# Performance work log

Hardware: AMD Instinct MI355X
Metric: run time of the kernel (lower is better)

The kernel has to match this reference:

```python
import jax, jax.numpy as jnp
import numpy as np

SHAPES = ((64, 64), (32, 32), (16, 16), (8, 8))
HEADS, LV, P = 8, 4, 8


def _ln(x, g, b, eps=1e-5):
    m = x.mean(-1, keepdims=True)
    v = ((x - m) ** 2).mean(-1, keepdims=True)
    return (x - m) * jax.lax.rsqrt(v + eps) * g + b


def _sample_level(v, H, W, loc):
    # v: [B, heads, H*W, hd] value for one level; loc: [B, L, heads, P, 2] in [0,1]
    # Matches F.grid_sample(mode='bilinear', padding_mode='zeros', align_corners=False)
    x = loc[..., 0] * W - 0.5
    y = loc[..., 1] * H - 0.5
    x0 = jnp.floor(x)
    y0 = jnp.floor(y)
    B, L, hds, Pn = x.shape
    acc = 0.0
    for dx, dy in ((0, 0), (1, 0), (0, 1), (1, 1)):
        xi = x0 + dx
        yi = y0 + dy
        w = (1.0 - jnp.abs(x - xi)) * (1.0 - jnp.abs(y - yi))
        valid = (xi >= 0) & (xi < W) & (yi >= 0) & (yi < H)
        idx = (jnp.clip(yi, 0, H - 1) * W + jnp.clip(xi, 0, W - 1)).astype(jnp.int32)
        idx_r = idx.transpose(0, 2, 1, 3).reshape(B, hds, L * Pn)  # [B,heads,L*P]
        g = jnp.take_along_axis(v, idx_r[..., None], axis=2)  # [B,heads,L*P,hd]
        g = g.reshape(B, hds, L, Pn, -1).transpose(0, 2, 1, 3, 4)  # [B,L,heads,P,hd]
        acc = acc + (w * valid.astype(w.dtype))[..., None] * g
    return acc


def setup_inputs() -> dict:
    key = jax.random.key(0)
    ks = iter(jax.random.split(key, 64))
    B, d, depth, dff = 2, 256, 6, 1024
    inp = {}
    for i, (H, W) in enumerate(SHAPES):
        inp[f"src{i}"] = jax.random.normal(next(ks), (B, d, H, W), jnp.float32)
        inp[f"pos{i}"] = jax.random.normal(next(ks), (B, d, H, W), jnp.float32)
    s = 0.02
    off_dim = HEADS * LV * P * 2  # 512
    aw_dim = HEADS * LV * P  # 256
    inp["level_embed"] = jax.random.normal(next(ks), (LV, d), jnp.float32)
    inp["W_off"] = jax.random.normal(next(ks), (depth, d, off_dim), jnp.float32) * s
    inp["b_off"] = jax.random.normal(next(ks), (depth, off_dim), jnp.float32) * 0.5
    inp["W_attn"] = jax.random.normal(next(ks), (depth, d, aw_dim), jnp.float32) * s
    inp["b_attn"] = jnp.zeros((depth, aw_dim), jnp.float32)
    inp["W_val"] = jax.random.normal(next(ks), (depth, d, d), jnp.float32) * s
    inp["b_val"] = jnp.zeros((depth, d), jnp.float32)
    inp["W_out"] = jax.random.normal(next(ks), (depth, d, d), jnp.float32) * s
    inp["b_out"] = jnp.zeros((depth, d), jnp.float32)
    inp["ln1_g"] = jnp.ones((depth, d), jnp.float32)
    inp["ln1_b"] = jnp.zeros((depth, d), jnp.float32)
    inp["W1"] = jax.random.normal(next(ks), (depth, d, dff), jnp.float32) * s
    inp["b1"] = jnp.zeros((depth, dff), jnp.float32)
    inp["W2"] = jax.random.normal(next(ks), (depth, dff, d), jnp.float32) * s
    inp["b2"] = jnp.zeros((depth, d), jnp.float32)
    inp["ln2_g"] = jnp.ones((depth, d), jnp.float32)
    inp["ln2_b"] = jnp.zeros((depth, d), jnp.float32)
    return inp


def reference(src0, src1, src2, src3, pos0, pos1, pos2, pos3, level_embed,
              W_off, b_off, W_attn, b_attn, W_val, b_val, W_out, b_out,
              ln1_g, ln1_b, W1, b1, W2, b2, ln2_g, ln2_b):
    srcs = [src0, src1, src2, src3]
    poss = [pos0, pos1, pos2, pos3]
    B, d = src0.shape[0], src0.shape[1]
    hd = d // HEADS
    # flatten multi-scale maps: [B, C, H, W] -> [B, H*W, C]
    src_flat = jnp.concatenate([s.reshape(B, d, -1).transpose(0, 2, 1) for s in srcs], 1)
    pos_flat = jnp.concatenate(
        [p.reshape(B, d, -1).transpose(0, 2, 1) + level_embed[i] for i, p in enumerate(poss)], 1)
    # reference points; masks are all-False so valid_ratios == 1 (same ref for every level)
    refs = []
    for (H, W) in SHAPES:
        gy, gx = jnp.meshgrid((jnp.arange(H) + 0.5) / H, (jnp.arange(W) + 0.5) / W, indexing='ij')
        refs.append(jnp.stack([gx.reshape(-1), gy.reshape(-1)], -1))
    ref = jnp.concatenate(refs, 0)  # [L, 2]
    norm = jnp.array([[W, H] for (H, W) in SHAPES], jnp.float32)  # [LV, 2] (W_, H_)
    sizes = [H * W for (H, W) in SHAPES]
    starts = np.cumsum([0] + sizes[:-1]).tolist()
    depth = W_off.shape[0]
    L = src_flat.shape[1]
    x = src_flat
    for i in range(depth):
        # pre-norm deformable self-attention; value comes from un-normed residual stream
        x2 = _ln(x, ln1_g[i], ln1_b[i])
        q = x2 + pos_flat
        off = (q @ W_off[i] + b_off[i]).reshape(B, L, HEADS, LV, P, 2)
        attn = jax.nn.softmax((q @ W_attn[i] + b_attn[i]).reshape(B, L, HEADS, LV * P), -1)
        attn = attn.reshape(B, L, HEADS, LV, P)
        val = (x @ W_val[i] + b_val[i]).reshape(B, L, HEADS, hd).transpose(0, 2, 1, 3)  # [B,heads,L,hd]
        loc = ref[None, :, None, None, None, :] + off / norm[None, None, None, :, None, :]
        out = 0.0
        for l, (H, W) in enumerate(SHAPES):
            vl = val[:, :, starts[l]:starts[l] + sizes[l]]
            sl = _sample_level(vl, H, W, loc[:, :, :, l])  # [B,L,heads,P,hd]
            out = out + (attn[:, :, :, l, :, None] * sl).sum(3)
        out = out.reshape(B, L, d) @ W_out[i] + b_out[i]
        x = x + out
        # pre-norm FFN with exact gelu (torch default)
        x2 = _ln(x, ln2_g[i], ln2_b[i])
        x = x + jax.nn.gelu(x2 @ W1[i] + b1[i], approximate=False) @ W2[i] + b2[i]
    return x
```

## Files before the change

kernel.cpp:

```cpp
#include <hip/hip_runtime.h>
#include <hip/hip_bf16.h>
#include <math.h>

#define L_TOK 5440
#define NTOK  10880
#define D     256

typedef __attribute__((ext_vector_type(8))) short short8;
typedef __attribute__((ext_vector_type(4))) short short4v;
typedef __attribute__((ext_vector_type(4))) float f32x4;

__device__ __forceinline__ short f2bf(float f) {
    __hip_bfloat16 h = __float2bfloat16(f);
    return __builtin_bit_cast(short, h);
}
__device__ __forceinline__ float bf2f(short s) {
    unsigned u = ((unsigned)(unsigned short)s) << 16;
    return __builtin_bit_cast(float, u);
}

#define GLL16(gp, lp) \
    __builtin_amdgcn_global_load_lds((const __attribute__((address_space(1))) void*)(gp), \
                                     (__attribute__((address_space(3))) void*)(lp), 16, 0, 0)

__global__ __launch_bounds__(256) void flat_kernel(
    const float* __restrict__ s, const float* __restrict__ p, const float* __restrict__ le,
    float* __restrict__ x, short* __restrict__ xb, float* __restrict__ pos,
    int HW, int start, int lv)
{
    __shared__ float ts[32][33], tp[32][33];
    int b = blockIdx.z, c0 = blockIdx.y * 32, pix0 = blockIdx.x * 32;
    int tx = threadIdx.x & 31, ty = threadIdx.x >> 5;
#pragma unroll
    for (int i = 0; i < 4; ++i) {
        int c = c0 + ty + i * 8;
        size_t gi = ((size_t)b * D + c) * HW + pix0 + tx;
        ts[ty + i * 8][tx] = s[gi];
        tp[ty + i * 8][tx] = p[gi];
    }
    __syncthreads();
#pragma unroll
    for (int i = 0; i < 4; ++i) {
        int pix = pix0 + ty + i * 8;
        size_t bl = (size_t)b * L_TOK + start + pix;
        int c = c0 + tx;
        float v = ts[tx][ty + i * 8];
        x[bl * D + c]   = v;
        xb[bl * D + c]  = f2bf(v);
        pos[bl * D + c] = tp[tx][ty + i * 8] + le[lv * D + c];
    }
}

__global__ __launch_bounds__(256) void wconv_kernel(
    const float* __restrict__ W, short* __restrict__ Wt, int K, int N,
    int dstride, int rowoff)
{
    __shared__ float tile[32][33];
    int d = blockIdx.z;
    int n0 = blockIdx.x * 32, k0 = blockIdx.y * 32;
    const float* Wd = W + (size_t)d * K * N;
    short* Wtd = Wt + (size_t)d * dstride + (size_t)rowoff * K;
    int tx = threadIdx.x & 31, ty = threadIdx.x >> 5;
#pragma unroll
    for (int i = 0; i < 4; ++i)
        tile[ty + i * 8][tx] = Wd[(size_t)(k0 + ty + i * 8) * N + n0 + tx];
    __syncthreads();
#pragma unroll
    for (int i = 0; i < 4; ++i)
        Wtd[(size_t)(n0 + ty + i * 8) * K + k0 + tx] = f2bf(tile[tx][ty + i * 8]);
}

__global__ __launch_bounds__(256) void bpack_kernel(
    const float* __restrict__ boff, const float* __restrict__ batt, float* __restrict__ bqa)
{
    int i = blockIdx.x * 256 + threadIdx.x;
    if (i >= 6 * 768) return;
    int d = i / 768, c = i - d * 768;
    bqa[i] = (c < 512) ? boff[d * 512 + c] : batt[d * 256 + c - 512];
}

__global__ __launch_bounds__(256) void ln_kernel(
    const float* __restrict__ x, const float* __restrict__ g, const float* __restrict__ bta,
    const float* __restrict__ pos, short* __restrict__ out)
{
    int wid = threadIdx.x >> 6, lane = threadIdx.x & 63;
    int m = blockIdx.x * 4 + wid;
    const float* xr = x + (size_t)m * D;
    float v[4];
#pragma unroll
    for (int i = 0; i < 4; ++i) v[i] = xr[lane + i * 64];
    float s = v[0] + v[1] + v[2] + v[3];
#pragma unroll
    for (int o = 32; o; o >>= 1) s += __shfl_xor(s, o);
    float mean = s * (1.0f / D);
    float sq = 0.0f;
#pragma unroll
    for (int i = 0; i < 4; ++i) { float d = v[i] - mean; sq += d * d; }
#pragma unroll
    for (int o = 32; o; o >>= 1) sq += __shfl_xor(sq, o);
    float rstd = rsqrtf(sq * (1.0f / D) + 1e-5f);
    short* orow = out + (size_t)m * D;
#pragma unroll
    for (int i = 0; i < 4; ++i) {
        int c = lane + i * 64;
        float o = (v[i] - mean) * rstd * g[c] + bta[c];
        if (pos) o += pos[(size_t)m * D + c];
        orow[c] = f2bf(o);
    }
}

__device__ __forceinline__ void mm_body(
    const short* __restrict__ A, const short* __restrict__ Wt,
    const float* __restrict__ bias, const float* __restrict__ resid,
    float* __restrict__ Cf, short* __restrict__ Cb,
    int row0, int col0, int K, int ldc, int act)
{
    __shared__ __align__(16) short As[128 * 64];
    __shared__ __align__(16) short Bs[128 * 64];
    int tid = threadIdx.x;
    int lane = tid & 63, w = tid >> 6;
    int wr = w >> 1, wc = w & 1;
    int l15 = lane & 15, l16 = lane >> 4;

    int a_off[4][2], b_off[4][2];
#pragma unroll
    for (int m = 0; m < 4; ++m) {
#pragma unroll
        for (int kk = 0; kk < 2; ++kk) {
            int ra = wr * 64 + m * 16 + l15;
            a_off[m][kk] = ra * 64 + (((kk * 4 + l16) ^ (ra & 7)) << 3);
            int rb = wc * 64 + m * 16 + l15;
            b_off[m][kk] = rb * 64 + (((kk * 4 + l16) ^ (rb & 7)) << 3);
        }
    }

    int sg = (lane & 7) ^ ((lane >> 3) & 7);
    const short* ag = A  + (size_t)(row0 + w * 32 + (lane >> 3)) * K + sg * 8;
    const short* bg = Wt + (size_t)(col0 + w * 32 + (lane >> 3)) * K + sg * 8;

    f32x4 acc[4][4];
#pragma unroll
    for (int m = 0; m < 4; ++m)
#pragma unroll
        for (int n = 0; n < 4; ++n) acc[m][n] = (f32x4){0.f, 0.f, 0.f, 0.f};

    for (int k0 = 0; k0 < K; k0 += 64) {
#pragma unroll
        for (int c = 0; c < 4; ++c) {
            GLL16(ag + (size_t)c * 8 * K + k0, &As[w * 2048 + c * 512]);
            GLL16(bg + (size_t)c * 8 * K + k0, &Bs[w * 2048 + c * 512]);
        }
        __syncthreads();
#pragma unroll
        for (int kk = 0; kk < 2; ++kk) {
            short8 af[4], bfr[4];
#pragma unroll
            for (int m = 0; m < 4; ++m) af[m] = *(short8*)&As[a_off[m][kk]];
#pragma unroll
            for (int n = 0; n < 4; ++n) bfr[n] = *(short8*)&Bs[b_off[n][kk]];
#pragma unroll
            for (int m = 0; m < 4; ++m)
#pragma unroll
                for (int n = 0; n < 4; ++n)
                    acc[m][n] = __builtin_amdgcn_mfma_f32_16x16x32_bf16(af[m], bfr[n], acc[m][n], 0, 0, 0);
        }
        __syncthreads();
    }

#pragma unroll
    for (int m = 0; m < 4; ++m) {
#pragma unroll
        for (int j = 0; j < 4; ++j) {
            int row = row0 + wr * 64 + m * 16 + l16 * 4 + j;
#pragma unroll
            for (int n = 0; n < 4; ++n) {
                int col = col0 + wc * 64 + n * 16 + l15;
                float v = acc[m][n][j] + bias[col];
                if (act) v = 0.5f * v * (1.0f + erff(v * 0.70710678118654752f));
                if (resid) v += resid[(size_t)row * ldc + col];
                if (Cf) Cf[(size_t)row * ldc + col] = v;
                if (Cb) Cb[(size_t)row * ldc + col] = f2bf(v);
            }
        }
    }
}

__global__ __launch_bounds__(256) void mm_kernel(
    const short* __restrict__ A, const short* __restrict__ Wt,
    const float* __restrict__ bias, const float* __restrict__ resid,
    float* __restrict__ Cf, short* __restrict__ Cb, int K, int ldc, int act)
{
    mm_body(A, Wt, bias, resid, Cf, Cb, blockIdx.y * 128, blockIdx.x * 128, K, ldc, act);
}

__global__ __launch_bounds__(256) void mm2_kernel(
    const short* __restrict__ A1, const short* __restrict__ Wt1, const float* __restrict__ bias1,
    float* __restrict__ Cf1, int ldc1,
    const short* __restrict__ A2, const short* __restrict__ Wt2, const float* __restrict__ bias2,
    short* __restrict__ Cb2, int ldc2,
    int nx1, int K)
{
    const short *A, *Wt; const float* bias; float* Cf; short* Cb; int ldc, col0;
    if ((int)blockIdx.x < nx1) {
        A = A1; Wt = Wt1; bias = bias1; Cf = Cf1; Cb = nullptr; ldc = ldc1;
        col0 = blockIdx.x * 128;
    } else {
        A = A2; Wt = Wt2; bias = bias2; Cf = nullptr; Cb = Cb2; ldc = ldc2;
        col0 = (blockIdx.x - nx1) * 128;
    }
    mm_body(A, Wt, bias, nullptr, Cf, Cb, blockIdx.y * 128, col0, K, ldc, 0);
}

__global__ __launch_bounds__(256) void sample_kernel(
    const float* __restrict__ big, const short* __restrict__ val, short* __restrict__ out)
{
    __shared__ float sw[8 * 132];
    __shared__ int   si[8 * 132];
    int bl = blockIdx.x;
    int b = bl / L_TOK, l = bl - b * L_TOK;
    const float* row = big + (size_t)bl * 768;
    int t = threadIdx.x;
    {
        int head = t >> 5, lvp = t & 31, lv = lvp >> 3, p = lvp & 7;
        int lq, r;
        if (l < 4096)      { lq = 0; r = l;        }
        else if (l < 5120) { lq = 1; r = l - 4096; }
        else if (l < 5376) { lq = 2; r = l - 5120; }
        else               { lq = 3; r = l - 5376; }
        int sh = 6 - lq;
        float invSq = 1.0f / (float)(1 << sh);
        float refx = ((r & ((1 << sh) - 1)) + 0.5f) * invSq;
        float refy = ((r >> sh) + 0.5f) * invSq;
        int S = 64 >> lv;
        int start = (lv == 0) ? 0 : (lv == 1) ? 4096 : (lv == 2) ? 5120 : 5376;
        float Sf = (float)S;
        float logit = row[512 + head * 32 + lvp];
        float mx = logit;
#pragma unroll
        for (int o = 16; o; o >>= 1) mx = fmaxf(mx, __shfl_xor(mx, o));
        float e = __expf(logit - mx);
        float ssum = e;
#pragma unroll
        for (int o = 16; o; o >>= 1) ssum += __shfl_xor(ssum, o);
        float a = e / ssum;
        float ox = row[head * 64 + lv * 16 + p * 2 + 0];
        float oy = row[head * 64 + lv * 16 + p * 2 + 1];
        float X = refx * Sf + ox - 0.5f;
        float Y = refy * Sf + oy - 0.5f;
        float x0 = floorf(X), y0 = floorf(Y);
        float fx = X - x0, fy = Y - y0;
        int xi0 = (int)x0, yi0 = (int)y0;
        int qt = lvp >> 3, sidx = lvp & 7;
        int base_w = head * 132 + qt * 33 + sidx * 4;
#pragma unroll
        for (int tap = 0; tap < 4; ++tap) {
            int dx = tap & 1, dy = tap >> 1;
            int xi = xi0 + dx, yi = yi0 + dy;
            float wgt = (dx ? fx : 1.0f - fx) * (dy ? fy : 1.0f - fy);
            bool valid = (xi >= 0) && (xi < S) && (yi >= 0) && (yi < S);
            int xc = xi < 0 ? 0 : (xi > S - 1 ? S - 1 : xi);
            int yc = yi < 0 ? 0 : (yi > S - 1 ? S - 1 : yi);
            sw[base_w + tap] = valid ? wgt * a : 0.0f;
            si[base_w + tap] = start + yc * S + xc;
        }
    }
    __syncthreads();
    int h = t >> 5, sgp = (t >> 2) & 7, cg = t & 3;
    const short* vb = val + (size_t)b * L_TOK * D + h * 32 + cg * 8;
    float a0 = 0.f, a1 = 0.f, a2 = 0.f, a3 = 0.f;
    float a4 = 0.f, a5 = 0.f, a6 = 0.f, a7 = 0.f;
#pragma unroll
    for (int ss = 0; ss < 4; ++ss) {
        int base = h * 132 + ss * 33 + sgp * 4;
#pragma unroll
        for (int tap = 0; tap < 4; ++tap) {
            float wgt = sw[base + tap];
            int   idx = si[base + tap];
            const short8 g = *(const short8*)&vb[(size_t)idx * D];
            a0 += wgt * bf2f(g[0]); a1 += wgt * bf2f(g[1]);
            a2 += wgt * bf2f(g[2]); a3 += wgt * bf2f(g[3]);
            a4 += wgt * bf2f(g[4]); a5 += wgt * bf2f(g[5]);
            a6 += wgt * bf2f(g[6]); a7 += wgt * bf2f(g[7]);
        }
    }
#pragma unroll
    for (int o = 4; o <= 16; o <<= 1) {
        a0 += __shfl_xor(a0, o); a1 += __shfl_xor(a1, o);
        a2 += __shfl_xor(a2, o); a3 += __shfl_xor(a3, o);
        a4 += __shfl_xor(a4, o); a5 += __shfl_xor(a5, o);
        a6 += __shfl_xor(a6, o); a7 += __shfl_xor(a7, o);
    }
    if (sgp == 0) {
        short8 o;
        o[0] = f2bf(a0); o[1] = f2bf(a1); o[2] = f2bf(a2); o[3] = f2bf(a3);
        o[4] = f2bf(a4); o[5] = f2bf(a5); o[6] = f2bf(a6); o[7] = f2bf(a7);
        *(short8*)&out[(size_t)bl * D + h * 32 + cg * 8] = o;
    }
}

extern "C" void kernel_launch(void* const* d_in, const int* in_sizes, int n_in,
                              void* d_out, int out_size, void* d_ws, size_t ws_size,
                              hipStream_t stream)
{
    const float* s0    = (const float*)d_in[0];
    const float* p0    = (const float*)d_in[1];
    const float* s1    = (const float*)d_in[2];
    const float* p1    = (const float*)d_in[3];
    const float* s2    = (const float*)d_in[4];
    const float* p2    = (const float*)d_in[5];
    const float* s3    = (const float*)d_in[6];
    const float* p3    = (const float*)d_in[7];
    const float* lvl   = (const float*)d_in[8];
    const float* W_off = (const float*)d_in[9];
    const float* b_off = (const float*)d_in[10];
    const float* W_att = (const float*)d_in[11];
    const float* b_att = (const float*)d_in[12];
    const float* W_val = (const float*)d_in[13];
    const float* b_val = (const float*)d_in[14];
    const float* W_out = (const float*)d_in[15];
    const float* b_out = (const float*)d_in[16];
    const float* ln1g  = (const float*)d_in[17];
    const float* ln1b  = (const float*)d_in[18];
    const float* W1    = (const float*)d_in[19];
    const float* b1    = (const float*)d_in[20];
    const float* W2    = (const float*)d_in[21];
    const float* b2    = (const float*)d_in[22];
    const float* ln2g  = (const float*)d_in[23];
    const float* ln2b  = (const float*)d_in[24];

    const size_t S1 = (size_t)NTOK * D;
    float* xbuf = (float*)d_ws;
    float* pos  = xbuf + S1;
    float* big  = pos + S1;
    float* bqa  = big + 3 * S1;
    short* qbf   = (short*)(bqa + 6 * 768);
    short* x_bf  = qbf + S1;
    short* valbf = x_bf + S1;
    short* sampb = valbf + S1;
    short* hidbf = sampb + S1;
    short* wt_qa  = hidbf + 4 * S1;
    short* wt_val = wt_qa  + (size_t)6 * 768 * 256;
    short* wt_out = wt_val + (size_t)6 * 256 * 256;
    short* wt_1   = wt_out + (size_t)6 * 256 * 256;
    short* wt_2   = wt_1   + (size_t)6 * 1024 * 256;

    wconv_kernel<<<dim3(16, 8, 6), 256, 0, stream>>>(W_off, wt_qa, 256, 512, 768 * 256, 0);
    wconv_kernel<<<dim3(8, 8, 6),  256, 0, stream>>>(W_att, wt_qa, 256, 256, 768 * 256, 512);
    wconv_kernel<<<dim3(8, 8, 6),  256, 0, stream>>>(W_val, wt_val, 256, 256, 256 * 256, 0);
    wconv_kernel<<<dim3(8, 8, 6),  256, 0, stream>>>(W_out, wt_out, 256, 256, 256 * 256, 0);
    wconv_kernel<<<dim3(32, 8, 6), 256, 0, stream>>>(W1,    wt_1,   256, 1024, 1024 * 256, 0);
    wconv_kernel<<<dim3(8, 32, 6), 256, 0, stream>>>(W2,    wt_2,   1024, 256, 256 * 1024, 0);
    bpack_kernel<<<18, 256, 0, stream>>>(b_off, b_att, bqa);

    flat_kernel<<<dim3(128, 8, 2), 256, 0, stream>>>(s0, p0, lvl, xbuf, x_bf, pos, 4096, 0, 0);
    flat_kernel<<<dim3(32, 8, 2),  256, 0, stream>>>(s1, p1, lvl, xbuf, x_bf, pos, 1024, 4096, 1);
    flat_kernel<<<dim3(8, 8, 2),   256, 0, stream>>>(s2, p2, lvl, xbuf, x_bf, pos, 256, 5120, 2);
    flat_kernel<<<dim3(2, 8, 2),   256, 0, stream>>>(s3, p3, lvl, xbuf, x_bf, pos, 64, 5376, 3);

    for (int i = 0; i < 6; ++i) {
        ln_kernel<<<NTOK / 4, 256, 0, stream>>>(xbuf, ln1g + i * 256, ln1b + i * 256, pos, qbf);
        mm2_kernel<<<dim3(8, 85), 256, 0, stream>>>(
            qbf, wt_qa + (size_t)i * 768 * 256, bqa + i * 768, big, 768,
            x_bf, wt_val + (size_t)i * 256 * 256, b_val + i * 256, valbf, 256,
            6, 256);
        sample_kernel<<<NTOK, 256, 0, stream>>>(big, valbf, sampb);
        mm_kernel<<<dim3(2, 85), 256, 0, stream>>>(
            sampb, wt_out + (size_t)i * 256 * 256, b_out + i * 256, xbuf, xbuf, nullptr, 256, 256, 0);
        ln_kernel<<<NTOK / 4, 256, 0, stream>>>(xbuf, ln2g + i * 256, ln2b + i * 256, nullptr, qbf);
        mm_kernel<<<dim3(8, 85), 256, 0, stream>>>(
            qbf, wt_1 + (size_t)i * 1024 * 256, b1 + i * 1024, nullptr, nullptr, hidbf, 256, 1024, 1);
        float* outp = (i == 5) ? (float*)d_out : xbuf;
        short* xbp  = (i == 5) ? nullptr : x_bf;
        mm_kernel<<<dim3(2, 85), 256, 0, stream>>>(
            hidbf, wt_2 + (size_t)i * 256 * 1024, b2 + i * 256, xbuf, outp, xbp, 1024, 256, 0);
    }
}
```

Before: 921.4 us.

## Shrink GEMM row tile to 64 and double-buffer LDS K-tiles

Replaces the 128x128 GEMM tile with a 64-row tile templated on column width (128 or 64), so each wave covers all 64 rows and a slice of columns. The grids grow to 170 row blocks, and the N=256 GEMMs get 4 column blocks, which raises block count for the 256-CU device. The K loop is now double-buffered in LDS: the next tile is staged while the current one is computed, with one barrier per iteration. The cost is less data reuse per block and more A/B reloads.

```diff
diff --git a/kernel.cpp b/kernel.cpp
--- a/kernel.cpp
+++ b/kernel.cpp
@@ -109,72 +109,90 @@
     }
 }
 
-__device__ __forceinline__ void mm_body(
+template<int BN>
+__device__ __forceinline__ void mm_body64(
     const short* __restrict__ A, const short* __restrict__ Wt,
     const float* __restrict__ bias, const float* __restrict__ resid,
     float* __restrict__ Cf, short* __restrict__ Cb,
     int row0, int col0, int K, int ldc, int act)
 {
-    __shared__ __align__(16) short As[128 * 64];
-    __shared__ __align__(16) short Bs[128 * 64];
-    int tid = threadIdx.x;
-    int lane = tid & 63, w = tid >> 6;
-    int wr = w >> 1, wc = w & 1;
+    constexpr int NW  = BN / 4;
+    constexpr int NF  = NW / 16;
+    constexpr int BCH = BN / 32;
+    __shared__ __align__(16) short As[2][64 * 64];
+    __shared__ __align__(16) short Bs[2][BN * 64];
+    int tid = threadIdx.x, lane = tid & 63, w = tid >> 6;
     int l15 = lane & 15, l16 = lane >> 4;
 
-    int a_off[4][2], b_off[4][2];
+    int a_off[4][2], b_off[NF][2];
+#pragma unroll
+    for (int m = 0; m < 4; ++m)
+#pragma unroll
+        for (int kk = 0; kk < 2; ++kk) {
+            int ra = m * 16 + l15;
+            a_off[m][kk] = ra * 64 + (((kk * 4 + l16) ^ (ra & 7)) << 3);
+        }
+#pragma unroll
+    for (int n = 0; n < NF; ++n)
+#pragma unroll
+        for (int kk = 0; kk < 2; ++kk) {
+            int rb = w * NW + n * 16 + l15;
+            b_off[n][kk] = rb * 64 + (((kk * 4 + l16) ^ (rb & 7)) << 3);
+        }
+
+    int sg = (lane & 7) ^ ((lane >> 3) & 7);
+    const short* ag = A  + (size_t)(row0 + w * 16 + (lane >> 3)) * K + sg * 8;
+    const short* bg = Wt + (size_t)(col0 + w * NW + (lane >> 3)) * K + sg * 8;
+
+    f32x4 acc[4][NF];
+#pragma unroll
+    for (int m = 0; m < 4; ++m)
+#pragma unroll
+        for (int n = 0; n < NF; ++n) acc[m][n] = (f32x4){0.f, 0.f, 0.f, 0.f};
+
+    auto stage = [&](int buf, int kofs) {
+#pragma unroll
+        for (int c = 0; c < 2; ++c)
+            GLL16(ag + (size_t)c * 8 * K + kofs, &As[buf][w * 1024 + c * 512]);
+#pragma unroll
+        for (int c = 0; c < BCH; ++c)
+            GLL16(bg + (size_t)c * 8 * K + kofs, &Bs[buf][w * NW * 64 + c * 512]);
+    };
+    auto comp = [&](int buf) {
+#pragma unroll
+        for (int kk = 0; kk < 2; ++kk) {
+            short8 af[4], bfr[NF];
+#pragma unroll
+            for (int m = 0; m < 4; ++m) af[m] = *(short8*)&As[buf][a_off[m][kk]];
+#pragma unroll
+            for (int n = 0; n < NF; ++n) bfr[n] = *(short8*)&Bs[buf][b_off[n][kk]];
+#pragma unroll
+            for (int m = 0; m < 4; ++m)
+#pragma unroll
+                for (int n = 0; n < NF; ++n)
+                    acc[m][n] = __builtin_amdgcn_mfma_f32_16x16x32_bf16(af[m], bfr[n], acc[m][n], 0, 0, 0);
+        }
+    };
+
+    stage(0, 0);
+    __syncthreads();
+    int cur = 0;
+    for (int k0 = 64; k0 < K; k0 += 64) {
+        stage(cur ^ 1, k0);
+        comp(cur);
+        __syncthreads();
+        cur ^= 1;
+    }
+    comp(cur);
+
 #pragma unroll
     for (int m = 0; m < 4; ++m) {
 #pragma unroll
-        for (int kk = 0; kk < 2; ++kk) {
-            int ra = wr * 64 + m * 16 + l15;
-            a_off[m][kk] = ra * 64 + (((kk * 4 + l16) ^ (ra & 7)) << 3);
-            int rb = wc * 64 + m * 16 + l15;
-            b_off[m][kk] = rb * 64 + (((kk * 4 + l16) ^ (rb & 7)) << 3);
-        }
-    }
-
-    int sg = (lane & 7) ^ ((lane >> 3) & 7);
-    const short* ag = A  + (size_t)(row0 + w * 32 + (lane >> 3)) * K + sg * 8;
-    const short* bg = Wt + (size_t)(col0 + w * 32 + (lane >> 3)) * K + sg * 8;
-
-    f32x4 acc[4][4];
-#pragma unroll
-    for (int m = 0; m < 4; ++m)
-#pragma unroll
-        for (int n = 0; n < 4; ++n) acc[m][n] = (f32x4){0.f, 0.f, 0.f, 0.f};
-
-    for (int k0 = 0; k0 < K; k0 += 64) {
-#pragma unroll
-        for (int c = 0; c < 4; ++c) {
-            GLL16(ag + (size_t)c * 8 * K + k0, &As[w * 2048 + c * 512]);
-            GLL16(bg + (size_t)c * 8 * K + k0, &Bs[w * 2048 + c * 512]);
-        }
-        __syncthreads();
-#pragma unroll
-        for (int kk = 0; kk < 2; ++kk) {
-            short8 af[4], bfr[4];
-#pragma unroll
-            for (int m = 0; m < 4; ++m) af[m] = *(short8*)&As[a_off[m][kk]];
-#pragma unroll
-            for (int n = 0; n < 4; ++n) bfr[n] = *(short8*)&Bs[b_off[n][kk]];
-#pragma unroll
-            for (int m = 0; m < 4; ++m)
-#pragma unroll
-                for (int n = 0; n < 4; ++n)
-                    acc[m][n] = __builtin_amdgcn_mfma_f32_16x16x32_bf16(af[m], bfr[n], acc[m][n], 0, 0, 0);
-        }
-        __syncthreads();
-    }
-
-#pragma unroll
-    for (int m = 0; m < 4; ++m) {
-#pragma unroll
         for (int j = 0; j < 4; ++j) {
-            int row = row0 + wr * 64 + m * 16 + l16 * 4 + j;
-#pragma unroll
-            for (int n = 0; n < 4; ++n) {
-                int col = col0 + wc * 64 + n * 16 + l15;
+            int row = row0 + m * 16 + l16 * 4 + j;
+#pragma unroll
+            for (int n = 0; n < NF; ++n) {
+                int col = col0 + w * NW + n * 16 + l15;
                 float v = acc[m][n][j] + bias[col];
                 if (act) v = 0.5f * v * (1.0f + erff(v * 0.70710678118654752f));
                 if (resid) v += resid[(size_t)row * ldc + col];
@@ -185,12 +203,13 @@
     }
 }
 
+template<int BN>
 __global__ __launch_bounds__(256) void mm_kernel(
     const short* __restrict__ A, const short* __restrict__ Wt,
     const float* __restrict__ bias, const float* __restrict__ resid,
     float* __restrict__ Cf, short* __restrict__ Cb, int K, int ldc, int act)
 {
-    mm_body(A, Wt, bias, resid, Cf, Cb, blockIdx.y * 128, blockIdx.x * 128, K, ldc, act);
+    mm_body64<BN>(A, Wt, bias, resid, Cf, Cb, blockIdx.y * 64, blockIdx.x * BN, K, ldc, act);
 }
 
 __global__ __launch_bounds__(256) void mm2_kernel(
@@ -208,7 +227,7 @@
         A = A2; Wt = Wt2; bias = bias2; Cf = nullptr; Cb = Cb2; ldc = ldc2;
         col0 = (blockIdx.x - nx1) * 128;
     }
-    mm_body(A, Wt, bias, nullptr, Cf, Cb, blockIdx.y * 128, col0, K, ldc, 0);
+    mm_body64<128>(A, Wt, bias, nullptr, Cf, Cb, blockIdx.y * 64, col0, K, ldc, 0);
 }
 
 __global__ __launch_bounds__(256) void sample_kernel(
@@ -359,19 +378,19 @@
 
     for (int i = 0; i < 6; ++i) {
         ln_kernel<<<NTOK / 4, 256, 0, stream>>>(xbuf, ln1g + i * 256, ln1b + i * 256, pos, qbf);
-        mm2_kernel<<<dim3(8, 85), 256, 0, stream>>>(
+        mm2_kernel<<<dim3(8, 170), 256, 0, stream>>>(
             qbf, wt_qa + (size_t)i * 768 * 256, bqa + i * 768, big, 768,
             x_bf, wt_val + (size_t)i * 256 * 256, b_val + i * 256, valbf, 256,
             6, 256);
         sample_kernel<<<NTOK, 256, 0, stream>>>(big, valbf, sampb);
-        mm_kernel<<<dim3(2, 85), 256, 0, stream>>>(
+        mm_kernel<64><<<dim3(4, 170), 256, 0, stream>>>(
             sampb, wt_out + (size_t)i * 256 * 256, b_out + i * 256, xbuf, xbuf, nullptr, 256, 256, 0);
         ln_kernel<<<NTOK / 4, 256, 0, stream>>>(xbuf, ln2g + i * 256, ln2b + i * 256, nullptr, qbf);
-        mm_kernel<<<dim3(8, 85), 256, 0, stream>>>(
+        mm_kernel<128><<<dim3(8, 170), 256, 0, stream>>>(
             qbf, wt_1 + (size_t)i * 1024 * 256, b1 + i * 1024, nullptr, nullptr, hidbf, 256, 1024, 1);
         float* outp = (i == 5) ? (float*)d_out : xbuf;
         short* xbp  = (i == 5) ? nullptr : x_bf;
-        mm_kernel<<<dim3(2, 85), 256, 0, stream>>>(
+        mm_kernel<64><<<dim3(4, 170), 256, 0, stream>>>(
             hidbf, wt_2 + (size_t)i * 256 * 1024, b2 + i * 256, xbuf, outp, xbp, 1024, 256, 0);
     }
 }
```

Result: faster. 793.6 us (-13.9%).
